# Performance work log

Measured on AMD Instinct MI355X. Metric: run time of the kernel, lower is better.

## Reference

```python
import jax, jax.numpy as jnp
import numpy as np

TOP_K_FRACTION = 0.1


def setup_inputs() -> dict:
    key = jax.random.key(0)
    k1, k2, k3 = jax.random.split(key, 3)
    B, H, S, D = 2, 12, 1024, 64
    q = jax.random.normal(k1, (B, H, S, D), dtype=jnp.float32)
    k = jax.random.normal(k2, (B, H, S, D), dtype=jnp.float32)
    v = jax.random.normal(k3, (B, H, S, D), dtype=jnp.float32)
    mask = jnp.zeros((B, 1, 1, S), dtype=jnp.float32)
    return {"q": q, "k": k, "v": v, "mask": mask}


def reference(q, k, v, mask):
    B, H, S, D = q.shape
    k_precise = max(1, int(S * TOP_K_FRACTION))
    # binary (sign) approximation of attention scores; detached like torch
    q_bin = jnp.sign(jax.lax.stop_gradient(q))
    k_bin = jnp.sign(jax.lax.stop_gradient(k))
    approx_scores = jnp.einsum('bhsd,bhtd->bhst', q_bin, k_bin) / D  # [B,H,S,S]
    _, topk_idx = jax.lax.top_k(approx_scores, k_precise)  # [B,H,S,kp]
    # gather top-k keys/values per query: [B,H,S,kp,D]
    k_gathered = jnp.take_along_axis(k[:, :, None, :, :], topk_idx[..., None], axis=3)
    v_gathered = jnp.take_along_axis(v[:, :, None, :, :], topk_idx[..., None], axis=3)
    scale = np.float32(1.0 / np.sqrt(D))
    precise_scores = jnp.einsum('bhsd,bhskd->bhsk', q, k_gathered) * scale
    # gather mask along key positions: mask [B,1,1,S] -> [B,H,S,kp]
    mask_gathered = jnp.take_along_axis(
        jnp.broadcast_to(mask, (B, H, S, S)), topk_idx, axis=-1)
    precise_scores = precise_scores + mask_gathered
    precise_probs = jax.nn.softmax(precise_scores, axis=-1)
    attn_output = jnp.einsum('bhsk,bhskd->bhsd', precise_probs, v_gathered)
    return attn_output
```

## Files before the change

kernel.cpp:

```cpp
#include <hip/hip_runtime.h>
#include <hip/hip_fp16.h>
#include <cstdint>

#define BB 2
#define HH 12
#define SS 1024
#define DD 64
#define KP 102
#define KPAD 104
#define QPB 4

typedef _Float16 half2v __attribute__((ext_vector_type(2)));
typedef _Float16 half8v __attribute__((ext_vector_type(8)));

template <int CTRL>
__device__ __forceinline__ float dpp_f(float x) {
    return __builtin_bit_cast(float,
        __builtin_amdgcn_update_dpp(0, __builtin_bit_cast(int, x), CTRL, 0xF, 0xF, false));
}
__device__ __forceinline__ float group8_sum(float x) {
    x += dpp_f<0xB1>(x);
    x += dpp_f<0x4E>(x);
    x += dpp_f<0x141>(x);
    return x;
}
__device__ __forceinline__ int mbcnt64(unsigned long long m) {
    return (int)__builtin_amdgcn_mbcnt_hi((unsigned)(m >> 32),
               __builtin_amdgcn_mbcnt_lo((unsigned)(m & 0xffffffffull), 0u));
}
__device__ __forceinline__ half2v shfl_xor_h2(half2v v, int m) {
    return __builtin_bit_cast(half2v, __shfl_xor(__builtin_bit_cast(int, v), m));
}

__global__ __launch_bounds__(256) void pack_kernel(
    const float* __restrict__ k, const float* __restrict__ v,
    unsigned long long* __restrict__ kbits, _Float16* __restrict__ kvh)
{
    int row  = (int)((blockIdx.x * 256 + threadIdx.x) >> 6);
    int lane = (int)(threadIdx.x & 63);
    if (row >= BB * HH * SS) return;
    float kv = k[(size_t)row * DD + lane];
    float vv = v[(size_t)row * DD + lane];
    unsigned long long km = __ballot(kv > 0.0f);
    kvh[(size_t)row * 128 + lane]      = (_Float16)kv;
    kvh[(size_t)row * 128 + 64 + lane] = (_Float16)vv;
    if (lane == 0) kbits[row] = km;
}

__global__ __launch_bounds__(256, 4) void battn_kernel(
    const float* __restrict__ q, const _Float16* __restrict__ kvh,
    const float* __restrict__ mask,
    const unsigned long long* __restrict__ kbits,
    float* __restrict__ out)
{
    const int tid  = (int)threadIdx.x;
    const int w    = tid >> 6;
    const int lane = tid & 63;
    const int query = (int)blockIdx.x * QPB + w;
    const int bh    = query >> 10;
    const int b     = bh / HH;

    __shared__ int sel_t[QPB][KPAD];

    const float qreg = q[(size_t)query * DD + lane];
    const unsigned long long qm = __ballot(qreg > 0.0f);

    const unsigned long long* kb = kbits + (size_t)bh * SS;
    int pbin[16];
    #pragma unroll
    for (int j = 0; j < 16; ++j)
        pbin[j] = (int)__popcll(qm ^ kb[j * 64 + lane]);

    #define COUNT_LE(P, OUTC)                                      \
        { int _c = 0;                                              \
          _Pragma("unroll")                                        \
          for (int j = 0; j < 16; ++j)                             \
              _c += (int)__popcll(__ballot(pbin[j] <= (P)));       \
          (OUTC) = _c; }
    int P = 27, c, clt;
    COUNT_LE(P, c);
    if (c >= KP) {
        COUNT_LE(P - 1, clt);
        while (clt >= KP) { c = clt; --P; COUNT_LE(P - 1, clt); }
    } else {
        do { clt = c; ++P; COUNT_LE(P, c); } while (c < KP);
    }
    const int binP = P;
    const int need = KP - clt;
    #undef COUNT_LE

    if (lane < KPAD - KP)
        sel_t[w][KP + lane] = 0;
    int base = 0, tie_base = 0;
    #pragma unroll
    for (int j = 0; j < 16; ++j) {
        bool isGt  = pbin[j] < binP;
        bool isTie = (pbin[j] == binP);
        unsigned long long tiem = __ballot(isTie);
        int rank = tie_base + mbcnt64(tiem);
        bool take = isGt || (isTie && rank < need);
        unsigned long long tm = __ballot(take);
        if (take)
            sel_t[w][base + mbcnt64(tm)] = j * 64 + lane;
        base     += (int)__popcll(tm);
        tie_base += (int)__popcll(tiem);
    }

    const int sub = lane & 7, g = lane >> 3;
    const float* qrow = q + (size_t)query * DD + sub * 8;
    half2v qh[4];
    #pragma unroll
    for (int d = 0; d < 4; ++d) {
        float2 f2 = *(const float2*)(qrow + d * 2);
        half2v h; h[0] = (_Float16)(f2.x * 0.125f); h[1] = (_Float16)(f2.y * 0.125f);
        qh[d] = h;
    }
    const _Float16* kvrows  = kvh + (size_t)bh * SS * 128;
    const float*    maskrow = mask + (size_t)b * SS;

    half2v acch[4];
    #pragma unroll
    for (int d = 0; d < 4; ++d) { acch[d][0] = (_Float16)0; acch[d][1] = (_Float16)0; }
    float l_part = 0.0f;

    #pragma unroll
    for (int ii = 0; ii < 13; ++ii) {
        const int i = ii * 8 + g;
        const int t = sel_t[w][i];
        const _Float16* p = kvrows + (size_t)t * 128 + sub * 8;
        half8v kv8 = *(const half8v*)p;
        half8v vv8 = *(const half8v*)(p + 64);
        half2v k0; k0[0] = kv8[0]; k0[1] = kv8[1];
        half2v k1; k1[0] = kv8[2]; k1[1] = kv8[3];
        half2v k2; k2[0] = kv8[4]; k2[1] = kv8[5];
        half2v k3; k3[0] = kv8[6]; k3[1] = kv8[7];
        float s = fmaf(maskrow[t], 0.125f, -0.5f);
        s = __builtin_amdgcn_fdot2(qh[0], k0, s, false);
        s = __builtin_amdgcn_fdot2(qh[1], k1, s, false);
        s = __builtin_amdgcn_fdot2(qh[2], k2, s, false);
        s = __builtin_amdgcn_fdot2(qh[3], k3, s, false);
        s = group8_sum(s);
        float e = __expf(s);
        if (ii == 12 && i >= KP) e = 0.0f;
        l_part += e;
        _Float16 eh = (_Float16)e;
        half2v e2; e2[0] = eh; e2[1] = eh;
        #pragma unroll
        for (int d = 0; d < 4; ++d) {
            half2v v2; v2[0] = vv8[d * 2]; v2[1] = vv8[d * 2 + 1];
            acch[d] = e2 * v2 + acch[d];
        }
    }

    float l = l_part;
    l += __shfl_xor(l, 8);
    l += __shfl_xor(l, 16);
    l += __shfl_xor(l, 32);
    #pragma unroll
    for (int d = 0; d < 4; ++d) {
        acch[d] = acch[d] + shfl_xor_h2(acch[d], 8);
        acch[d] = acch[d] + shfl_xor_h2(acch[d], 16);
        acch[d] = acch[d] + shfl_xor_h2(acch[d], 32);
    }
    if (lane < 8) {
        const float rinv = __frcp_rn(l);
        float* orow = out + (size_t)query * DD + lane * 8;
        float4 o0 = make_float4((float)acch[0][0] * rinv, (float)acch[0][1] * rinv,
                                (float)acch[1][0] * rinv, (float)acch[1][1] * rinv);
        float4 o1 = make_float4((float)acch[2][0] * rinv, (float)acch[2][1] * rinv,
                                (float)acch[3][0] * rinv, (float)acch[3][1] * rinv);
        *(float4*)orow       = o0;
        *(float4*)(orow + 4) = o1;
    }
}

extern "C" void kernel_launch(void* const* d_in, const int* in_sizes, int n_in,
                              void* d_out, int out_size, void* d_ws, size_t ws_size,
                              hipStream_t stream) {
    const float* q    = (const float*)d_in[0];
    const float* k    = (const float*)d_in[1];
    const float* v    = (const float*)d_in[2];
    const float* mask = (const float*)d_in[3];
    float* out = (float*)d_out;

    const int rows = BB * HH * SS;
    unsigned long long* kbits = (unsigned long long*)d_ws;
    _Float16* kvh = (_Float16*)((char*)d_ws + (size_t)rows * sizeof(unsigned long long));

    pack_kernel<<<(rows * 64 + 255) / 256, 256, 0, stream>>>(k, v, kbits, kvh);
    battn_kernel<<<rows / QPB, 256, 0, stream>>>(q, kvh, mask, kbits, out);
}
```

Baseline: 109.4 us.

## Replace sparse gather attention with dense MFMA attention masked by top-k bitmask

Instead of gathering the 102 selected K/V rows per query, the kernel now builds a per-query selection bitmask and computes dense QK^T and PV over all 1024 keys for a 64-query tile using 16x16x32 fp16 MFMA, zeroing the probabilities of keys that were not selected. K and a transposed V are staged through LDS in 128-key chunks, and the pack kernel now writes V transposed. This trades the random-gather memory traffic for roughly ten times more arithmetic, done on matrix cores with coalesced loads. The softmax uses a constant offset in place of a max, so very large scores could overflow, and the transposed V write in the pack kernel is strided.

```diff
diff --git a/kernel.cpp b/kernel.cpp
--- a/kernel.cpp
+++ b/kernel.cpp
@@ -7,171 +7,202 @@
 #define SS 1024
 #define DD 64
 #define KP 102
-#define KPAD 104
-#define QPB 4
-
-typedef _Float16 half2v __attribute__((ext_vector_type(2)));
-typedef _Float16 half8v __attribute__((ext_vector_type(8)));
-
+#define QT 64
+#define CHK 128
+#define NCHUNK 8
+#define KROW 72
+#define VROW 136
+
+typedef _Float16 half8v  __attribute__((ext_vector_type(8)));
+typedef float    float4v __attribute__((ext_vector_type(4)));
+typedef unsigned long long u64;
+
+__device__ __forceinline__ int mbcnt64(u64 m) {
+    return (int)__builtin_amdgcn_mbcnt_hi((unsigned)(m >> 32),
+               __builtin_amdgcn_mbcnt_lo((unsigned)(m & 0xffffffffull), 0u));
+}
 template <int CTRL>
 __device__ __forceinline__ float dpp_f(float x) {
     return __builtin_bit_cast(float,
         __builtin_amdgcn_update_dpp(0, __builtin_bit_cast(int, x), CTRL, 0xF, 0xF, false));
 }
-__device__ __forceinline__ float group8_sum(float x) {
+__device__ __forceinline__ float row16_sum(float x) {
     x += dpp_f<0xB1>(x);
     x += dpp_f<0x4E>(x);
     x += dpp_f<0x141>(x);
+    x += dpp_f<0x140>(x);
     return x;
-}
-__device__ __forceinline__ int mbcnt64(unsigned long long m) {
-    return (int)__builtin_amdgcn_mbcnt_hi((unsigned)(m >> 32),
-               __builtin_amdgcn_mbcnt_lo((unsigned)(m & 0xffffffffull), 0u));
-}
-__device__ __forceinline__ half2v shfl_xor_h2(half2v v, int m) {
-    return __builtin_bit_cast(half2v, __shfl_xor(__builtin_bit_cast(int, v), m));
 }
 
 __global__ __launch_bounds__(256) void pack_kernel(
     const float* __restrict__ k, const float* __restrict__ v,
-    unsigned long long* __restrict__ kbits, _Float16* __restrict__ kvh)
+    u64* __restrict__ kbits, _Float16* __restrict__ kh, _Float16* __restrict__ vT)
 {
     int row  = (int)((blockIdx.x * 256 + threadIdx.x) >> 6);
     int lane = (int)(threadIdx.x & 63);
     if (row >= BB * HH * SS) return;
     float kv = k[(size_t)row * DD + lane];
     float vv = v[(size_t)row * DD + lane];
-    unsigned long long km = __ballot(kv > 0.0f);
-    kvh[(size_t)row * 128 + lane]      = (_Float16)kv;
-    kvh[(size_t)row * 128 + 64 + lane] = (_Float16)vv;
+    u64 km = __ballot(kv > 0.0f);
+    kh[(size_t)row * DD + lane] = (_Float16)kv;
+    int bh = row >> 10, t = row & (SS - 1);
+    vT[((size_t)bh * DD + lane) * SS + t] = (_Float16)vv;
     if (lane == 0) kbits[row] = km;
 }
 
-__global__ __launch_bounds__(256, 4) void battn_kernel(
-    const float* __restrict__ q, const _Float16* __restrict__ kvh,
-    const float* __restrict__ mask,
-    const unsigned long long* __restrict__ kbits,
-    float* __restrict__ out)
+__global__ __launch_bounds__(256, 2) void battn_kernel(
+    const float* __restrict__ q, const _Float16* __restrict__ kh,
+    const _Float16* __restrict__ vT, const float* __restrict__ mask,
+    const u64* __restrict__ kbits, float* __restrict__ out)
 {
     const int tid  = (int)threadIdx.x;
     const int w    = tid >> 6;
     const int lane = tid & 63;
-    const int query = (int)blockIdx.x * QPB + w;
-    const int bh    = query >> 10;
-    const int b     = bh / HH;
-
-    __shared__ int sel_t[QPB][KPAD];
-
-    const float qreg = q[(size_t)query * DD + lane];
-    const unsigned long long qm = __ballot(qreg > 0.0f);
-
-    const unsigned long long* kb = kbits + (size_t)bh * SS;
-    int pbin[16];
-    #pragma unroll
-    for (int j = 0; j < 16; ++j)
-        pbin[j] = (int)__popcll(qm ^ kb[j * 64 + lane]);
-
-    #define COUNT_LE(P, OUTC)                                      \
-        { int _c = 0;                                              \
-          _Pragma("unroll")                                        \
-          for (int j = 0; j < 16; ++j)                             \
-              _c += (int)__popcll(__ballot(pbin[j] <= (P)));       \
-          (OUTC) = _c; }
-    int P = 27, c, clt;
-    COUNT_LE(P, c);
-    if (c >= KP) {
-        COUNT_LE(P - 1, clt);
-        while (clt >= KP) { c = clt; --P; COUNT_LE(P - 1, clt); }
-    } else {
-        do { clt = c; ++P; COUNT_LE(P, c); } while (c < KP);
-    }
-    const int binP = P;
-    const int need = KP - clt;
-    #undef COUNT_LE
-
-    if (lane < KPAD - KP)
-        sel_t[w][KP + lane] = 0;
-    int base = 0, tie_base = 0;
-    #pragma unroll
-    for (int j = 0; j < 16; ++j) {
-        bool isGt  = pbin[j] < binP;
-        bool isTie = (pbin[j] == binP);
-        unsigned long long tiem = __ballot(isTie);
-        int rank = tie_base + mbcnt64(tiem);
-        bool take = isGt || (isTie && rank < need);
-        unsigned long long tm = __ballot(take);
-        if (take)
-            sel_t[w][base + mbcnt64(tm)] = j * 64 + lane;
-        base     += (int)__popcll(tm);
-        tie_base += (int)__popcll(tiem);
-    }
-
-    const int sub = lane & 7, g = lane >> 3;
-    const float* qrow = q + (size_t)query * DD + sub * 8;
-    half2v qh[4];
-    #pragma unroll
-    for (int d = 0; d < 4; ++d) {
-        float2 f2 = *(const float2*)(qrow + d * 2);
-        half2v h; h[0] = (_Float16)(f2.x * 0.125f); h[1] = (_Float16)(f2.y * 0.125f);
-        qh[d] = h;
-    }
-    const _Float16* kvrows  = kvh + (size_t)bh * SS * 128;
-    const float*    maskrow = mask + (size_t)b * SS;
-
-    half2v acch[4];
-    #pragma unroll
-    for (int d = 0; d < 4; ++d) { acch[d][0] = (_Float16)0; acch[d][1] = (_Float16)0; }
-    float l_part = 0.0f;
-
-    #pragma unroll
-    for (int ii = 0; ii < 13; ++ii) {
-        const int i = ii * 8 + g;
-        const int t = sel_t[w][i];
-        const _Float16* p = kvrows + (size_t)t * 128 + sub * 8;
-        half8v kv8 = *(const half8v*)p;
-        half8v vv8 = *(const half8v*)(p + 64);
-        half2v k0; k0[0] = kv8[0]; k0[1] = kv8[1];
-        half2v k1; k1[0] = kv8[2]; k1[1] = kv8[3];
-        half2v k2; k2[0] = kv8[4]; k2[1] = kv8[5];
-        half2v k3; k3[0] = kv8[6]; k3[1] = kv8[7];
-        float s = fmaf(maskrow[t], 0.125f, -0.5f);
-        s = __builtin_amdgcn_fdot2(qh[0], k0, s, false);
-        s = __builtin_amdgcn_fdot2(qh[1], k1, s, false);
-        s = __builtin_amdgcn_fdot2(qh[2], k2, s, false);
-        s = __builtin_amdgcn_fdot2(qh[3], k3, s, false);
-        s = group8_sum(s);
-        float e = __expf(s);
-        if (ii == 12 && i >= KP) e = 0.0f;
-        l_part += e;
-        _Float16 eh = (_Float16)e;
-        half2v e2; e2[0] = eh; e2[1] = eh;
-        #pragma unroll
-        for (int d = 0; d < 4; ++d) {
-            half2v v2; v2[0] = vv8[d * 2]; v2[1] = vv8[d * 2 + 1];
-            acch[d] = e2 * v2 + acch[d];
-        }
-    }
-
-    float l = l_part;
-    l += __shfl_xor(l, 8);
-    l += __shfl_xor(l, 16);
-    l += __shfl_xor(l, 32);
-    #pragma unroll
-    for (int d = 0; d < 4; ++d) {
-        acch[d] = acch[d] + shfl_xor_h2(acch[d], 8);
-        acch[d] = acch[d] + shfl_xor_h2(acch[d], 16);
-        acch[d] = acch[d] + shfl_xor_h2(acch[d], 32);
-    }
-    if (lane < 8) {
-        const float rinv = __frcp_rn(l);
-        float* orow = out + (size_t)query * DD + lane * 8;
-        float4 o0 = make_float4((float)acch[0][0] * rinv, (float)acch[0][1] * rinv,
-                                (float)acch[1][0] * rinv, (float)acch[1][1] * rinv);
-        float4 o1 = make_float4((float)acch[2][0] * rinv, (float)acch[2][1] * rinv,
-                                (float)acch[3][0] * rinv, (float)acch[3][1] * rinv);
-        *(float4*)orow       = o0;
-        *(float4*)(orow + 4) = o1;
-    }
+    const int bh    = (int)blockIdx.x >> 4;
+    const int qtile = (int)blockIdx.x & 15;
+    const int bidx  = bh / HH;
+    const int qr    = lane & 15;
+    const int quad  = lane >> 4;
+
+    __shared__ __align__(16) _Float16 K_lds[CHK * KROW];
+    __shared__ __align__(16) _Float16 VT_lds[DD * VROW];
+    __shared__ __align__(16) _Float16 P_lds[4][16 * VROW];
+    __shared__ u64  selmask[QT][16];
+    __shared__ __align__(16) float mask_lds[SS];
+
+    {
+        const float* mrow = mask + (size_t)bidx * SS;
+        float4v mv = *(const float4v*)(mrow + tid * 4);
+        mv[0] -= 4.0f; mv[1] -= 4.0f; mv[2] -= 4.0f; mv[3] -= 4.0f;
+        *(float4v*)(&mask_lds[tid * 4]) = mv;
+    }
+
+    const u64* kb = kbits + (size_t)bh * SS;
+    u64 kbreg[16];
+    #pragma unroll
+    for (int j = 0; j < 16; ++j) kbreg[j] = kb[j * 64 + lane];
+    const float* qwave = q + ((size_t)bh * SS + qtile * QT + w * 16) * DD;
+
+    #pragma unroll 1
+    for (int qq = 0; qq < 16; ++qq) {
+        float qv = qwave[qq * DD + lane];
+        u64 qm = __ballot(qv > 0.0f);
+        int pbin[16];
+        #pragma unroll
+        for (int j = 0; j < 16; ++j) pbin[j] = (int)__popcll(qm ^ kbreg[j]);
+        #define COUNT_LE(P, OUTC)                                      \
+            { int _c = 0;                                              \
+              _Pragma("unroll")                                        \
+              for (int j = 0; j < 16; ++j)                             \
+                  _c += (int)__popcll(__ballot(pbin[j] <= (P)));       \
+              (OUTC) = _c; }
+        int P = 27, c, clt;
+        COUNT_LE(P, c);
+        if (c >= KP) {
+            COUNT_LE(P - 1, clt);
+            while (clt >= KP) { c = clt; --P; COUNT_LE(P - 1, clt); }
+        } else {
+            do { clt = c; ++P; COUNT_LE(P, c); } while (c < KP);
+        }
+        const int binP = P;
+        const int need = KP - clt;
+        #undef COUNT_LE
+        u64 my_tm = 0; int tie_base = 0;
+        #pragma unroll
+        for (int j = 0; j < 16; ++j) {
+            bool isGt  = pbin[j] < binP;
+            bool isTie = (pbin[j] == binP);
+            u64 tiem = __ballot(isTie);
+            int rank = tie_base + mbcnt64(tiem);
+            bool take = isGt || (isTie && rank < need);
+            u64 tm = __ballot(take);
+            if (lane == j) my_tm = tm;
+            tie_base += (int)__popcll(tiem);
+        }
+        if (lane < 16) selmask[w * 16 + qq][lane] = my_tm;
+    }
+
+    half8v qa0, qa1;
+    {
+        const float* qf = qwave + qr * DD + quad * 8;
+        #pragma unroll
+        for (int j = 0; j < 8; ++j) {
+            qa0[j] = (_Float16)(qf[j] * 0.125f);
+            qa1[j] = (_Float16)(qf[32 + j] * 0.125f);
+        }
+    }
+
+    const _Float16* khead  = kh + (size_t)bh * SS * DD;
+    const _Float16* vthead = vT + (size_t)bh * DD * SS;
+
+    float4v acc[4];
+    #pragma unroll
+    for (int dt = 0; dt < 4; ++dt) { acc[dt][0]=0.f; acc[dt][1]=0.f; acc[dt][2]=0.f; acc[dt][3]=0.f; }
+    float lp[4] = {0.f, 0.f, 0.f, 0.f};
+
+    #pragma unroll 1
+    for (int ch = 0; ch < NCHUNK; ++ch) {
+        __syncthreads();
+        #pragma unroll
+        for (int it = 0; it < 4; ++it) {
+            int s = tid + it * 256;
+            int row = s >> 3, c8 = s & 7;
+            *(half8v*)(&K_lds[row * KROW + c8 * 8]) =
+                *(const half8v*)(khead + (size_t)(ch * CHK + row) * DD + c8 * 8);
+        }
+        #pragma unroll
+        for (int it = 0; it < 4; ++it) {
+            int s = tid + it * 256;
+            int d = s >> 4, c8 = s & 15;
+            *(half8v*)(&VT_lds[d * VROW + c8 * 8]) =
+                *(const half8v*)(vthead + (size_t)d * SS + ch * CHK + c8 * 8);
+        }
+        __syncthreads();
+
+        #pragma unroll
+        for (int nt = 0; nt < 8; ++nt) {
+            const _Float16* kl = &K_lds[(nt * 16 + qr) * KROW + quad * 8];
+            half8v b0 = *(const half8v*)kl;
+            half8v b1 = *(const half8v*)(kl + 32);
+            float4v cfr; cfr[0]=0.f; cfr[1]=0.f; cfr[2]=0.f; cfr[3]=0.f;
+            cfr = __builtin_amdgcn_mfma_f32_16x16x32_f16(qa0, b0, cfr, 0, 0, 0);
+            cfr = __builtin_amdgcn_mfma_f32_16x16x32_f16(qa1, b1, cfr, 0, 0, 0);
+            const int tg   = ch * CHK + nt * 16 + qr;
+            const float mk = mask_lds[tg];
+            const int w32  = tg >> 5, b32 = tg & 31;
+            #pragma unroll
+            for (int r = 0; r < 4; ++r) {
+                unsigned sm = ((const unsigned*)selmask[w * 16 + quad * 4 + r])[w32];
+                float e = ((sm >> b32) & 1u) ? __expf(cfr[r] + mk) : 0.0f;
+                lp[r] += e;
+                P_lds[w][(quad * 4 + r) * VROW + nt * 16 + qr] = (_Float16)e;
+            }
+        }
+
+        half8v pa0 = *(const half8v*)(&P_lds[w][qr * VROW +  0 + quad * 8]);
+        half8v pa1 = *(const half8v*)(&P_lds[w][qr * VROW + 32 + quad * 8]);
+        half8v pa2 = *(const half8v*)(&P_lds[w][qr * VROW + 64 + quad * 8]);
+        half8v pa3 = *(const half8v*)(&P_lds[w][qr * VROW + 96 + quad * 8]);
+        #pragma unroll
+        for (int dt = 0; dt < 4; ++dt) {
+            const _Float16* vl = &VT_lds[(dt * 16 + qr) * VROW + quad * 8];
+            acc[dt] = __builtin_amdgcn_mfma_f32_16x16x32_f16(pa0, *(const half8v*)(vl +  0), acc[dt], 0, 0, 0);
+            acc[dt] = __builtin_amdgcn_mfma_f32_16x16x32_f16(pa1, *(const half8v*)(vl + 32), acc[dt], 0, 0, 0);
+            acc[dt] = __builtin_amdgcn_mfma_f32_16x16x32_f16(pa2, *(const half8v*)(vl + 64), acc[dt], 0, 0, 0);
+            acc[dt] = __builtin_amdgcn_mfma_f32_16x16x32_f16(pa3, *(const half8v*)(vl + 96), acc[dt], 0, 0, 0);
+        }
+    }
+
+    float rinv[4];
+    #pragma unroll
+    for (int r = 0; r < 4; ++r) rinv[r] = __frcp_rn(row16_sum(lp[r]));
+
+    float* orow = out + ((size_t)bh * SS + qtile * QT + w * 16) * DD;
+    #pragma unroll
+    for (int dt = 0; dt < 4; ++dt)
+        #pragma unroll
+        for (int r = 0; r < 4; ++r)
+            orow[(quad * 4 + r) * DD + dt * 16 + qr] = acc[dt][r] * rinv[r];
 }
 
 extern "C" void kernel_launch(void* const* d_in, const int* in_sizes, int n_in,
@@ -184,9 +215,10 @@
     float* out = (float*)d_out;
 
     const int rows = BB * HH * SS;
-    unsigned long long* kbits = (unsigned long long*)d_ws;
-    _Float16* kvh = (_Float16*)((char*)d_ws + (size_t)rows * sizeof(unsigned long long));
-
-    pack_kernel<<<(rows * 64 + 255) / 256, 256, 0, stream>>>(k, v, kbits, kvh);
-    battn_kernel<<<rows / QPB, 256, 0, stream>>>(q, kvh, mask, kbits, out);
-}
+    u64* kbits = (u64*)d_ws;
+    _Float16* kh = (_Float16*)((char*)d_ws + (size_t)rows * sizeof(u64));
+    _Float16* vT = kh + (size_t)rows * DD;
+
+    pack_kernel<<<(rows * 64 + 255) / 256, 256, 0, stream>>>(k, v, kbits, kh, vT);
+    battn_kernel<<<BB * HH * (SS / QT), 256, 0, stream>>>(q, kh, vT, mask, kbits, out);
+}
```

Measured after the change: 131.1 us. 1.2x slower.
